# Kernel optimization log

Hardware: AMD Instinct MI355X
Metric: run time of the kernel (lower is better)

Reference implementation:

```python
import jax, jax.numpy as jnp
import numpy as np

C, H, W = 4, 84, 84
T, B = 64, 32
HID = 512
ZD = 64
SLOPE = 0.01  # nn.LeakyReLU default


def setup_inputs() -> dict:
    key = jax.random.key(0)
    ks = jax.random.split(key, 16)
    f32 = jnp.float32

    def n(k, shape, scale):
        return jax.random.normal(k, shape, f32) * scale

    return {
        "x": jax.random.normal(ks[0], (T * B, C, H, W), f32),
        "done": (jax.random.uniform(ks[1], (T * B,)) < 0.05).astype(f32),
        "h0": jnp.zeros((B, HID), f32),
        "c0": jnp.zeros((B, HID), f32),
        "conv1_w": n(ks[2], (C, C, 5, 5), 0.15),
        "conv1_b": jnp.zeros((C,), f32),
        "conv2_w": n(ks[3], (C, C, 3, 3), 0.2),
        "conv2_b": jnp.zeros((C,), f32),
        "conv3_w": n(ks[4], (C, C, 3, 3), 0.2),
        "conv3_b": jnp.zeros((C,), f32),
        "fc1_w": n(ks[5], (HID, C * H * W), 0.01),
        "fc1_b": jnp.zeros((HID,), f32),
        "fc2_w": n(ks[6], (HID, HID), 0.05),
        "fc2_b": jnp.zeros((HID,), f32),
        "w_ih": n(ks[7], (4 * HID, HID), 0.04),
        "w_hh": n(ks[8], (4 * HID, HID), 0.04),
        "b_ih": jnp.zeros((4 * HID,), f32),
        "b_hh": jnp.zeros((4 * HID,), f32),
        "df_w": n(ks[9], (128, HID), 0.05),
        "df_b": jnp.zeros((128,), f32),
        "disc_w": n(ks[10], (ZD, 128), 0.01),
        "disc_b": jnp.zeros((ZD,), f32),
    }


def _lrelu(x):
    return jax.nn.leaky_relu(x, SLOPE)


def _conv(x, w, b):
    y = jax.lax.conv_general_dilated(
        x, w, window_strides=(1, 1), padding="SAME",
        dimension_numbers=("NCHW", "OIHW", "NCHW"))
    return _lrelu(y + b[None, :, None, None])


def reference(x, done, h0, c0, conv1_w, conv1_b, conv2_w, conv2_b, conv3_w,
              conv3_b, fc1_w, fc1_b, fc2_w, fc2_b, w_ih, w_hh, b_ih, b_hh,
              df_w, df_b, disc_w, disc_b):
    # conv + MLP feature extractor (self.network)
    h = _conv(x, conv1_w, conv1_b)
    h = _conv(h, conv2_w, conv2_b)
    h = _conv(h, conv3_w, conv3_b)
    h = h.reshape(h.shape[0], -1)                      # [T*B, C*H*W]
    h = _lrelu(h @ fc1_w.T + fc1_b)
    h = _lrelu(h @ fc2_w.T + fc2_b)                    # [T*B, 512]

    # env_first=False path: reshape to [T, B, 512]
    hid = h.reshape(T, B, HID)
    d = done.reshape(T, B)

    def step(carry, xs):
        hp, cp = carry
        xt, dt = xs
        mask = (1.0 - dt)[:, None]                     # done-based state reset
        hp = hp * mask
        cp = cp * mask
        gates = xt @ w_ih.T + b_ih + hp @ w_hh.T + b_hh  # [B, 4*HID], order i,f,g,o
        i, f, g, o = jnp.split(gates, 4, axis=-1)
        c = jax.nn.sigmoid(f) * cp + jax.nn.sigmoid(i) * jnp.tanh(g)
        hn = jax.nn.sigmoid(o) * jnp.tanh(c)
        return (hn, c), hn

    (hN, cN), ys = jax.lax.scan(step, (h0, c0), (hid, d))
    feat = ys.reshape(T * B, HID)

    disc_feat = _lrelu(feat @ df_w.T + df_b)           # [T*B, 128]
    logits = disc_feat @ disc_w.T + disc_b             # [T*B, z_dim]
    return logits, hN, cN
```

## Files before the change

### kernel.cpp

```cpp
#include <hip/hip_runtime.h>
#include <math.h>

#define SLOPE 0.01f

typedef __attribute__((ext_vector_type(8))) short bf16x8;
typedef __attribute__((ext_vector_type(4))) float f32x4;
typedef unsigned short ushort_t;

__device__ __forceinline__ float lrelu(float x) {
    return x > 0.f ? x : SLOPE * x;
}

__device__ __forceinline__ unsigned short f2bf(float f) {
    unsigned int u = __float_as_uint(f);
    u += 0x7fffu + ((u >> 16) & 1u);
    return (unsigned short)(u >> 16);
}

__device__ __forceinline__ float bf2f(unsigned short u) {
    return __uint_as_float((unsigned int)u << 16);
}

__global__ void cvt_bf16_kernel(const float* __restrict__ src,
                                unsigned short* __restrict__ dst, int n4) {
    int i = blockIdx.x * blockDim.x + threadIdx.x;
    if (i >= n4) return;
    float4 v = ((const float4*)src)[i];
    uint2 o;
    o.x = (unsigned)f2bf(v.x) | ((unsigned)f2bf(v.y) << 16);
    o.y = (unsigned)f2bf(v.z) | ((unsigned)f2bf(v.w) << 16);
    ((uint2*)dst)[i] = o;
}

template<int K, bool INBF, bool OUTBF>
__global__ __launch_bounds__(256) void conv_tile_kernel(
        const void* __restrict__ in_v,
        const float* __restrict__ w,
        const float* __restrict__ b,
        void* __restrict__ out_v) {
    constexpr int HALO = K / 2;
    constexpr int TILE_H = 12;
    constexpr int SH = TILE_H + 2 * HALO;
    constexpr int SW = 88;
    __shared__ float smem[4][SH][SW];

    int tid = threadIdx.x;
    int n = blockIdx.x;
    int row0 = blockIdx.y * TILE_H;
    const size_t imgOff = (size_t)n * (4 * 84 * 84);

    for (int it = tid; it < 4 * SH * 22; it += 256) {
        int item = it % 22;
        int rr = it / 22;
        int r = rr % SH;
        int ci = rr / SH;
        int gr = row0 + r - HALO;
        bool rv = (unsigned)gr < 84u;
        if (item < 21) {
            int gc = item * 4;
            float4 v = make_float4(0.f, 0.f, 0.f, 0.f);
            if (rv) {
                size_t off = imgOff + ((size_t)ci * 84 + gr) * 84 + gc;
                if (INBF) {
                    unsigned long long u =
                        *(const unsigned long long*)((const ushort_t*)in_v + off);
                    v.x = bf2f((unsigned short)u);
                    v.y = bf2f((unsigned short)(u >> 16));
                    v.z = bf2f((unsigned short)(u >> 32));
                    v.w = bf2f((unsigned short)(u >> 48));
                } else {
                    v = *(const float4*)((const float*)in_v + off);
                }
            }
            smem[ci][r][HALO + gc + 0] = v.x;
            smem[ci][r][HALO + gc + 1] = v.y;
            smem[ci][r][HALO + gc + 2] = v.z;
            smem[ci][r][HALO + gc + 3] = v.w;
        } else {
            if (HALO == 2) {
                smem[ci][r][0] = 0.f; smem[ci][r][1] = 0.f;
                smem[ci][r][86] = 0.f; smem[ci][r][87] = 0.f;
            } else {
                smem[ci][r][0] = 0.f;
                smem[ci][r][85] = 0.f; smem[ci][r][86] = 0.f; smem[ci][r][87] = 0.f;
            }
        }
    }
    __syncthreads();

    if (tid >= 252) return;
    int r  = tid / 21;
    int w0 = (tid % 21) * 4;

    float acc[4][4];
    #pragma unroll
    for (int co = 0; co < 4; ++co) {
        float bv = b[co];
        #pragma unroll
        for (int dw = 0; dw < 4; ++dw) acc[co][dw] = bv;
    }

    #pragma unroll
    for (int ci = 0; ci < 4; ++ci) {
        #pragma unroll
        for (int kh = 0; kh < K; ++kh) {
            float vals[K + 3];
            float4 v0 = *(const float4*)&smem[ci][r + kh][w0];
            vals[0] = v0.x; vals[1] = v0.y; vals[2] = v0.z; vals[3] = v0.w;
            if (K == 5) {
                float4 v1 = *(const float4*)&smem[ci][r + kh][w0 + 4];
                vals[4] = v1.x; vals[5] = v1.y; vals[6] = v1.z; vals[7] = v1.w;
            } else {
                float2 v1 = *(const float2*)&smem[ci][r + kh][w0 + 4];
                vals[4] = v1.x; vals[5] = v1.y;
            }
            #pragma unroll
            for (int co = 0; co < 4; ++co) {
                #pragma unroll
                for (int kw = 0; kw < K; ++kw) {
                    float wv = w[((co * 4 + ci) * K + kh) * K + kw];
                    #pragma unroll
                    for (int dw = 0; dw < 4; ++dw)
                        acc[co][dw] += vals[kw + dw] * wv;
                }
            }
        }
    }

    int oh = row0 + r;
    #pragma unroll
    for (int co = 0; co < 4; ++co) {
        size_t off = imgOff + ((size_t)co * 84 + oh) * 84 + w0;
        float o0 = lrelu(acc[co][0]);
        float o1 = lrelu(acc[co][1]);
        float o2 = lrelu(acc[co][2]);
        float o3 = lrelu(acc[co][3]);
        if (OUTBF) {
            uint2 p;
            p.x = (unsigned)f2bf(o0) | ((unsigned)f2bf(o1) << 16);
            p.y = (unsigned)f2bf(o2) | ((unsigned)f2bf(o3) << 16);
            *(uint2*)((ushort_t*)out_v + off) = p;
        } else {
            *(float4*)((float*)out_v + off) = make_float4(o0, o1, o2, o3);
        }
    }
}

template<bool DO_LRELU, bool BIAS2, bool OUTBF>
__global__ void gemm_bf16_kernel(const unsigned short* __restrict__ A,
                                 const unsigned short* __restrict__ B,
                                 const float* __restrict__ bias,
                                 const float* __restrict__ bias2,
                                 void* __restrict__ Cout,
                                 int M, int N, int K) {
    __shared__ unsigned short As[64][40];
    __shared__ unsigned short Bs[64][40];
    int tid = threadIdx.x;
    int rowBase = blockIdx.y * 64;
    int colBase = blockIdx.x * 64;

    int wave = tid >> 6;
    int l    = tid & 63;
    int wr = wave >> 1, wc = wave & 1;
    int lane16 = l & 15;
    int kb = (l >> 4) * 8;

    int sr = tid >> 2;
    int sk = (tid & 3) << 3;
    const unsigned short* Ap = A + (size_t)(rowBase + sr) * K + sk;
    const unsigned short* Bp = B + (size_t)(colBase + sr) * K + sk;

    f32x4 acc[2][2] = {};

    for (int k0 = 0; k0 < K; k0 += 32) {
        float4 av = *(const float4*)(Ap + k0);
        float4 bv = *(const float4*)(Bp + k0);
        __syncthreads();
        *(float4*)(&As[sr][sk]) = av;
        *(float4*)(&Bs[sr][sk]) = bv;
        __syncthreads();
        bf16x8 a0 = *(const bf16x8*)(&As[wr * 32 + lane16][kb]);
        bf16x8 a1 = *(const bf16x8*)(&As[wr * 32 + 16 + lane16][kb]);
        bf16x8 b0 = *(const bf16x8*)(&Bs[wc * 32 + lane16][kb]);
        bf16x8 b1 = *(const bf16x8*)(&Bs[wc * 32 + 16 + lane16][kb]);
        acc[0][0] = __builtin_amdgcn_mfma_f32_16x16x32_bf16(a0, b0, acc[0][0], 0, 0, 0);
        acc[0][1] = __builtin_amdgcn_mfma_f32_16x16x32_bf16(a0, b1, acc[0][1], 0, 0, 0);
        acc[1][0] = __builtin_amdgcn_mfma_f32_16x16x32_bf16(a1, b0, acc[1][0], 0, 0, 0);
        acc[1][1] = __builtin_amdgcn_mfma_f32_16x16x32_bf16(a1, b1, acc[1][1], 0, 0, 0);
    }

    int crow0 = rowBase + wr * 32 + (l >> 4) * 4;
    int ccol0 = colBase + wc * 32 + lane16;
    float bsv[2];
    #pragma unroll
    for (int j = 0; j < 2; ++j) {
        bsv[j] = bias[ccol0 + j * 16];
        if (BIAS2) bsv[j] += bias2[ccol0 + j * 16];
    }
    #pragma unroll
    for (int i = 0; i < 2; ++i) {
        #pragma unroll
        for (int r = 0; r < 4; ++r) {
            int row = crow0 + i * 16 + r;
            #pragma unroll
            for (int j = 0; j < 2; ++j) {
                float v = acc[i][j][r] + bsv[j];
                if (DO_LRELU) v = lrelu(v);
                size_t off = (size_t)row * N + ccol0 + j * 16;
                if (OUTBF) ((unsigned short*)Cout)[off] = f2bf(v);
                else       ((float*)Cout)[off] = v;
            }
        }
    }
}

__global__ void gemm_bf16_splitk_kernel(const unsigned short* __restrict__ A,
                                        const unsigned short* __restrict__ B,
                                        float* __restrict__ part,
                                        int M, int N, int K, int kChunk) {
    __shared__ unsigned short As[64][40];
    __shared__ unsigned short Bs[64][40];
    int tid = threadIdx.x;
    int rowBase = blockIdx.y * 64;
    int colBase = blockIdx.x * 64;
    int s = blockIdx.z;
    int kStart = s * kChunk;
    int kEnd = kStart + kChunk;

    int wave = tid >> 6;
    int l    = tid & 63;
    int wr = wave >> 1, wc = wave & 1;
    int lane16 = l & 15;
    int kb = (l >> 4) * 8;

    int sr = tid >> 2;
    int sk = (tid & 3) << 3;
    const unsigned short* Ap = A + (size_t)(rowBase + sr) * K + sk;
    const unsigned short* Bp = B + (size_t)(colBase + sr) * K + sk;

    f32x4 acc[2][2] = {};

    for (int k0 = kStart; k0 < kEnd; k0 += 32) {
        float4 av = *(const float4*)(Ap + k0);
        float4 bv = *(const float4*)(Bp + k0);
        __syncthreads();
        *(float4*)(&As[sr][sk]) = av;
        *(float4*)(&Bs[sr][sk]) = bv;
        __syncthreads();
        bf16x8 a0 = *(const bf16x8*)(&As[wr * 32 + lane16][kb]);
        bf16x8 a1 = *(const bf16x8*)(&As[wr * 32 + 16 + lane16][kb]);
        bf16x8 b0 = *(const bf16x8*)(&Bs[wc * 32 + lane16][kb]);
        bf16x8 b1 = *(const bf16x8*)(&Bs[wc * 32 + 16 + lane16][kb]);
        acc[0][0] = __builtin_amdgcn_mfma_f32_16x16x32_bf16(a0, b0, acc[0][0], 0, 0, 0);
        acc[0][1] = __builtin_amdgcn_mfma_f32_16x16x32_bf16(a0, b1, acc[0][1], 0, 0, 0);
        acc[1][0] = __builtin_amdgcn_mfma_f32_16x16x32_bf16(a1, b0, acc[1][0], 0, 0, 0);
        acc[1][1] = __builtin_amdgcn_mfma_f32_16x16x32_bf16(a1, b1, acc[1][1], 0, 0, 0);
    }

    float* Cp = part + (size_t)s * M * N;
    int crow0 = rowBase + wr * 32 + (l >> 4) * 4;
    int ccol0 = colBase + wc * 32 + lane16;
    #pragma unroll
    for (int i = 0; i < 2; ++i)
        #pragma unroll
        for (int r = 0; r < 4; ++r) {
            int row = crow0 + i * 16 + r;
            #pragma unroll
            for (int j = 0; j < 2; ++j)
                Cp[(size_t)row * N + ccol0 + j * 16] = acc[i][j][r];
        }
}

template<int S>
__global__ void splitk_reduce_kernel(const float* __restrict__ part,
                                     const float* __restrict__ bias,
                                     unsigned short* __restrict__ out,
                                     int MN, int N) {
    int i4 = blockIdx.x * blockDim.x + threadIdx.x;
    if (i4 * 4 >= MN) return;
    float4 acc = ((const float4*)part)[i4];
    #pragma unroll
    for (int s = 1; s < S; ++s) {
        float4 p = ((const float4*)(part + (size_t)s * MN))[i4];
        acc.x += p.x; acc.y += p.y; acc.z += p.z; acc.w += p.w;
    }
    int col4 = i4 % (N / 4);
    float4 bv = ((const float4*)bias)[col4];
    float o0 = lrelu(acc.x + bv.x);
    float o1 = lrelu(acc.y + bv.y);
    float o2 = lrelu(acc.z + bv.z);
    float o3 = lrelu(acc.w + bv.w);
    uint2 p;
    p.x = (unsigned)f2bf(o0) | ((unsigned)f2bf(o1) << 16);
    p.y = (unsigned)f2bf(o2) | ((unsigned)f2bf(o3) << 16);
    ((uint2*)out)[i4] = p;
}

__global__ void lstm_init_kernel(const float* __restrict__ h0,
                                 unsigned short* __restrict__ HA,
                                 int* __restrict__ bar) {
    int i = blockIdx.x * blockDim.x + threadIdx.x;
    if (i < 16384) HA[i] = f2bf(h0[i]);
    if (i < 64) bar[i] = 0;
}

__global__ __launch_bounds__(256, 1) void lstm_scan_kernel(
        const unsigned short* __restrict__ whh_b,
        const unsigned short* __restrict__ wih_b,
        const float* __restrict__ bih,
        const float* __restrict__ bhh,
        const unsigned short* __restrict__ HA,
        const float* __restrict__ c0,
        const unsigned short* __restrict__ hfc2,
        const float* __restrict__ done,
        unsigned short* __restrict__ feat,
        float* __restrict__ hN, float* __restrict__ cN,
        int* __restrict__ bar) {
    __shared__ float mds[2048];
    __shared__ float Gs[4][16][17];
    __shared__ unsigned short Hs[16][520];
    __shared__ unsigned short Xh[16][520];

    int tid = threadIdx.x;
    int jt = blockIdx.x >> 1;
    int bt = blockIdx.x & 1;

    for (int i = tid; i < 2048; i += 256) mds[i] = 1.0f - done[i];

    int g = tid >> 6;
    int l = tid & 63;
    int lane16 = l & 15;
    int khi = l >> 4;
    const unsigned short* Wp =
        whh_b + ((size_t)g * 512 + jt * 16 + lane16) * 512 + khi * 8;
    const unsigned short* Wxp =
        wih_b + ((size_t)g * 512 + jt * 16 + lane16) * 512 + khi * 8;
    bf16x8 wreg[16], wxreg[16];
    #pragma unroll
    for (int kk = 0; kk < 16; ++kk) {
        wreg[kk]  = *(const bf16x8*)(Wp + kk * 32);
        wxreg[kk] = *(const bf16x8*)(Wxp + kk * 32);
    }

    int jloc = tid & 15;
    int bloc = tid >> 4;
    int j = jt * 16 + jloc;
    int b = bt * 16 + bloc;
    float c_reg = c0[b * 512 + j];
    float bsv[4];
    #pragma unroll
    for (int gg = 0; gg < 4; ++gg)
        bsv[gg] = bih[gg * 512 + j] + bhh[gg * 512 + j];

    int* mybar = bar + bt * 32;

    {
        const float4* h4 = (const float4*)(HA + bt * 8192);
        const float4* x4 = (const float4*)(hfc2 + bt * 8192);
        #pragma unroll
        for (int u0 = 0; u0 < 4; ++u0) {
            int u = tid + u0 * 256;
            float4 hv = h4[u];
            float4 xv = x4[u];
            *(float4*)&Hs[u >> 6][(u & 63) * 8] = hv;
            *(float4*)&Xh[u >> 6][(u & 63) * 8] = xv;
        }
    }
    __syncthreads();

    for (int t = 0; t < 64; ++t) {
        f32x4 hacc0 = {}, hacc1 = {}, xacc0 = {}, xacc1 = {};
        #pragma unroll
        for (int kk = 0; kk < 16; kk += 2) {
            bf16x8 hb0 = *(const bf16x8*)(&Hs[lane16][khi * 8 + kk * 32]);
            bf16x8 hb1 = *(const bf16x8*)(&Hs[lane16][khi * 8 + kk * 32 + 32]);
            bf16x8 xb0 = *(const bf16x8*)(&Xh[lane16][khi * 8 + kk * 32]);
            bf16x8 xb1 = *(const bf16x8*)(&Xh[lane16][khi * 8 + kk * 32 + 32]);
            hacc0 = __builtin_amdgcn_mfma_f32_16x16x32_bf16(wreg[kk],      hb0, hacc0, 0, 0, 0);
            hacc1 = __builtin_amdgcn_mfma_f32_16x16x32_bf16(wreg[kk + 1],  hb1, hacc1, 0, 0, 0);
            xacc0 = __builtin_amdgcn_mfma_f32_16x16x32_bf16(wxreg[kk],     xb0, xacc0, 0, 0, 0);
            xacc1 = __builtin_amdgcn_mfma_f32_16x16x32_bf16(wxreg[kk + 1], xb1, xacc1, 0, 0, 0);
        }
        f32x4 hacc = hacc0 + hacc1;
        f32x4 xacc = xacc0 + xacc1;
        float mcol = mds[t * 32 + bt * 16 + lane16];
        #pragma unroll
        for (int r = 0; r < 4; ++r)
            Gs[g][khi * 4 + r][lane16] = xacc[r] + mcol * hacc[r];
        __syncthreads();

        float4 xv0, xv1, xv2, xv3;
        if (t < 63) {
            const float4* x4 =
                (const float4*)(hfc2 + (size_t)(t + 1) * 16384 + bt * 8192);
            xv0 = x4[tid];
            xv1 = x4[tid + 256];
            xv2 = x4[tid + 512];
            xv3 = x4[tid + 768];
        }

        int row = t * 32 + b;
        float m = mds[row];
        float ai = bsv[0] + Gs[0][jloc][bloc];
        float af = bsv[1] + Gs[1][jloc][bloc];
        float ag = bsv[2] + Gs[2][jloc][bloc];
        float ao = bsv[3] + Gs[3][jloc][bloc];
        float cp = c_reg * m;
        float si = 1.f / (1.f + __expf(-ai));
        float sf = 1.f / (1.f + __expf(-af));
        float so = 1.f / (1.f + __expf(-ao));
        c_reg = sf * cp + si * tanhf(ag);
        float hn = so * tanhf(c_reg);
        feat[(size_t)row * 512 + j] = f2bf(hn);
        if (t == 63) {
            hN[b * 512 + j] = hn;
            cN[b * 512 + j] = c_reg;
        }

        if (t < 63) {
            *(float4*)&Xh[tid >> 6][(tid & 63) * 8] = xv0;
            {
                int u = tid + 256;
                *(float4*)&Xh[u >> 6][(u & 63) * 8] = xv1;
                u = tid + 512;
                *(float4*)&Xh[u >> 6][(u & 63) * 8] = xv2;
                u = tid + 768;
                *(float4*)&Xh[u >> 6][(u & 63) * 8] = xv3;
            }
            __syncthreads();
            if (tid == 0) {
                int target = (t + 1) * 32;
                __hip_atomic_fetch_add(mybar, 1, __ATOMIC_ACQ_REL,
                                       __HIP_MEMORY_SCOPE_AGENT);
                while (__hip_atomic_load(mybar, __ATOMIC_RELAXED,
                                         __HIP_MEMORY_SCOPE_AGENT) < target)
                    __builtin_amdgcn_s_sleep(2);
                __builtin_amdgcn_fence(__ATOMIC_ACQUIRE, "agent");
            }
            __syncthreads();
            const float4* h4 =
                (const float4*)(feat + (size_t)t * 16384 + bt * 8192);
            #pragma unroll
            for (int u0 = 0; u0 < 4; ++u0) {
                int u = tid + u0 * 256;
                float4 hv = h4[u];
                *(float4*)&Hs[u >> 6][(u & 63) * 8] = hv;
            }
            __syncthreads();
        }
    }
}

extern "C" void kernel_launch(void* const* d_in, const int* in_sizes, int n_in,
                              void* d_out, int out_size, void* d_ws, size_t ws_size,
                              hipStream_t stream) {
    const float* x    = (const float*)d_in[0];
    const float* done = (const float*)d_in[1];
    const float* h0   = (const float*)d_in[2];
    const float* c0   = (const float*)d_in[3];
    const float* c1w  = (const float*)d_in[4];
    const float* c1b  = (const float*)d_in[5];
    const float* c2w  = (const float*)d_in[6];
    const float* c2b  = (const float*)d_in[7];
    const float* c3w  = (const float*)d_in[8];
    const float* c3b  = (const float*)d_in[9];
    const float* fc1w = (const float*)d_in[10];
    const float* fc1b = (const float*)d_in[11];
    const float* fc2w = (const float*)d_in[12];
    const float* fc2b = (const float*)d_in[13];
    const float* wih  = (const float*)d_in[14];
    const float* whh  = (const float*)d_in[15];
    const float* bih  = (const float*)d_in[16];
    const float* bhh  = (const float*)d_in[17];
    const float* dfw  = (const float*)d_in[18];
    const float* dfb  = (const float*)d_in[19];
    const float* dw   = (const float*)d_in[20];
    const float* db   = (const float*)d_in[21];
    float* out = (float*)d_out;

    const size_t CONV_ELEMS = 57802752;
    char* S = (char*)d_ws;
    unsigned short* c1out  = (unsigned short*)S;   S += CONV_ELEMS * 2;
    unsigned short* c2out  = (unsigned short*)S;   S += CONV_ELEMS * 2;
    unsigned short* c3out  = (unsigned short*)S;   S += CONV_ELEMS * 2;
    unsigned short* fc1w_b = (unsigned short*)S;   S += 28901376;
    unsigned short* fc2w_b = (unsigned short*)S;   S += 524288;
    unsigned short* wih_b  = (unsigned short*)S;   S += 2097152;
    unsigned short* whh_b  = (unsigned short*)S;   S += 2097152;
    unsigned short* dfw_b  = (unsigned short*)S;   S += 131072;
    unsigned short* dw_b   = (unsigned short*)S;   S += 16384;
    unsigned short* hfc1_b = (unsigned short*)S;   S += 2097152;
    unsigned short* hfc2_b = (unsigned short*)S;   S += 2097152;
    unsigned short* feat_b = (unsigned short*)S;   S += 2097152;
    unsigned short* dfeat_b= (unsigned short*)S;   S += 524288;
    unsigned short* HA     = (unsigned short*)S;   S += 32768;
    float*          part   = (float*)S;            S += 37748736;
    int*            bar    = (int*)S;              S += 256;

    dim3 cgrid(2048, 7);
    conv_tile_kernel<5, false, true><<<cgrid, 256, 0, stream>>>(x,     c1w, c1b, c1out);
    conv_tile_kernel<3, true,  true><<<cgrid, 256, 0, stream>>>(c1out, c2w, c2b, c2out);
    conv_tile_kernel<3, true,  true><<<cgrid, 256, 0, stream>>>(c2out, c3w, c3b, c3out);

    auto cvt = [&](const float* s, unsigned short* d, int n) {
        int n4 = n / 4;
        cvt_bf16_kernel<<<(n4 + 255) / 256, 256, 0, stream>>>(s, d, n4);
    };
    cvt(fc1w, fc1w_b, 14450688);
    cvt(fc2w, fc2w_b, 262144);
    cvt(wih,  wih_b,  1048576);
    cvt(whh,  whh_b,  1048576);
    cvt(dfw,  dfw_b,  65536);
    cvt(dw,   dw_b,   8192);

    gemm_bf16_splitk_kernel<<<dim3(8, 32, 9), 256, 0, stream>>>(
        c3out, fc1w_b, part, 2048, 512, 28224, 3136);
    splitk_reduce_kernel<9><<<dim3(1024), 256, 0, stream>>>(
        part, fc1b, hfc1_b, 1048576, 512);

    gemm_bf16_kernel<true, false, true><<<dim3(8, 32), 256, 0, stream>>>(
        hfc1_b, fc2w_b, fc2b, nullptr, hfc2_b, 2048, 512, 512);

    lstm_init_kernel<<<dim3(64), 256, 0, stream>>>(h0, HA, bar);
    lstm_scan_kernel<<<dim3(64), 256, 0, stream>>>(
        whh_b, wih_b, bih, bhh, HA, c0, hfc2_b, done, feat_b,
        out + 131072, out + 131072 + 16384, bar);

    gemm_bf16_kernel<true, false, true><<<dim3(2, 32), 256, 0, stream>>>(
        feat_b, dfw_b, dfb, nullptr, dfeat_b, 2048, 128, 512);
    gemm_bf16_kernel<false, false, false><<<dim3(1, 32), 256, 0, stream>>>(
        dfeat_b, dw_b, db, nullptr, out, 2048, 64, 128);
}
```

Before: 837.0 us.

## Fuse conv2 and conv3 into one tiled kernel and merge weight conversions

```diff
diff --git a/kernel.cpp b/kernel.cpp
--- a/kernel.cpp
+++ b/kernel.cpp
@@ -21,11 +21,23 @@
     return __uint_as_float((unsigned int)u << 16);
 }
 
-__global__ void cvt_bf16_kernel(const float* __restrict__ src,
-                                unsigned short* __restrict__ dst, int n4) {
+__global__ void cvt_all_kernel(const float* __restrict__ s0,
+                               const float* __restrict__ s1,
+                               const float* __restrict__ s2,
+                               const float* __restrict__ s3,
+                               const float* __restrict__ s4,
+                               const float* __restrict__ s5,
+                               unsigned short* __restrict__ dst) {
     int i = blockIdx.x * blockDim.x + threadIdx.x;
-    if (i >= n4) return;
-    float4 v = ((const float4*)src)[i];
+    if (i >= 4220928) return;
+    const float* src; int base;
+    if (i < 3612672)      { src = s0; base = 0; }
+    else if (i < 3678208) { src = s1; base = 3612672; }
+    else if (i < 3940352) { src = s2; base = 3678208; }
+    else if (i < 4202496) { src = s3; base = 3940352; }
+    else if (i < 4218880) { src = s4; base = 4202496; }
+    else                  { src = s5; base = 4218880; }
+    float4 v = ((const float4*)src)[i - base];
     uint2 o;
     o.x = (unsigned)f2bf(v.x) | ((unsigned)f2bf(v.y) << 16);
     o.y = (unsigned)f2bf(v.z) | ((unsigned)f2bf(v.w) << 16);
@@ -142,6 +154,139 @@
             *(uint2*)((ushort_t*)out_v + off) = p;
         } else {
             *(float4*)((float*)out_v + off) = make_float4(o0, o1, o2, o3);
+        }
+    }
+}
+
+__global__ __launch_bounds__(384) void conv23_fused_kernel(
+        const ushort_t* __restrict__ in_b,
+        const float* __restrict__ w2, const float* __restrict__ b2,
+        const float* __restrict__ w3, const float* __restrict__ b3,
+        unsigned short* __restrict__ out) {
+    __shared__ float ins[4][18][88];
+    __shared__ float mid[4][16][88];
+
+    int tid = threadIdx.x;
+    int n = blockIdx.x;
+    int r0 = blockIdx.y * 14;
+    const size_t imgOff = (size_t)n * (4 * 84 * 84);
+
+    for (int it = tid; it < 4 * 18 * 22; it += 384) {
+        int item = it % 22;
+        int rr = it / 22;
+        int r = rr % 18;
+        int ci = rr / 18;
+        int gr = r0 - 2 + r;
+        bool rv = (unsigned)gr < 84u;
+        if (item < 21) {
+            int gc = item * 4;
+            float4 v = make_float4(0.f, 0.f, 0.f, 0.f);
+            if (rv) {
+                unsigned long long u = *(const unsigned long long*)
+                    (in_b + imgOff + ((size_t)ci * 84 + gr) * 84 + gc);
+                v.x = bf2f((unsigned short)u);
+                v.y = bf2f((unsigned short)(u >> 16));
+                v.z = bf2f((unsigned short)(u >> 32));
+                v.w = bf2f((unsigned short)(u >> 48));
+            }
+            ins[ci][r][1 + gc + 0] = v.x;
+            ins[ci][r][1 + gc + 1] = v.y;
+            ins[ci][r][1 + gc + 2] = v.z;
+            ins[ci][r][1 + gc + 3] = v.w;
+        } else {
+            ins[ci][r][0] = 0.f;
+            ins[ci][r][85] = 0.f; ins[ci][r][86] = 0.f; ins[ci][r][87] = 0.f;
+        }
+    }
+    __syncthreads();
+
+    if (tid < 128) {
+        int co = tid >> 5; int rr = (tid & 31) >> 1; int cc = (tid & 1) ? 85 : 0;
+        mid[co][rr][cc] = 0.f;
+    }
+    if (tid < 336) {
+        int m  = tid / 21;
+        int c0 = (tid % 21) * 4;
+        int gm = r0 - 1 + m;
+        float acc[4][4];
+        #pragma unroll
+        for (int co = 0; co < 4; ++co) {
+            float bv = b2[co];
+            #pragma unroll
+            for (int dw = 0; dw < 4; ++dw) acc[co][dw] = bv;
+        }
+        #pragma unroll
+        for (int ci = 0; ci < 4; ++ci) {
+            #pragma unroll
+            for (int kh = 0; kh < 3; ++kh) {
+                float vals[6];
+                float4 v0 = *(const float4*)&ins[ci][m + kh][c0];
+                float2 v1 = *(const float2*)&ins[ci][m + kh][c0 + 4];
+                vals[0] = v0.x; vals[1] = v0.y; vals[2] = v0.z; vals[3] = v0.w;
+                vals[4] = v1.x; vals[5] = v1.y;
+                #pragma unroll
+                for (int co = 0; co < 4; ++co) {
+                    #pragma unroll
+                    for (int kw = 0; kw < 3; ++kw) {
+                        float wv = w2[((co * 4 + ci) * 3 + kh) * 3 + kw];
+                        #pragma unroll
+                        for (int dw = 0; dw < 4; ++dw)
+                            acc[co][dw] += vals[kw + dw] * wv;
+                    }
+                }
+            }
+        }
+        bool valid = (unsigned)gm < 84u;
+        #pragma unroll
+        for (int co = 0; co < 4; ++co)
+            #pragma unroll
+            for (int dw = 0; dw < 4; ++dw)
+                mid[co][m][1 + c0 + dw] = valid ? lrelu(acc[co][dw]) : 0.f;
+    }
+    __syncthreads();
+
+    if (tid < 294) {
+        int ro = tid / 21;
+        int c0 = (tid % 21) * 4;
+        float acc[4][4];
+        #pragma unroll
+        for (int co = 0; co < 4; ++co) {
+            float bv = b3[co];
+            #pragma unroll
+            for (int dw = 0; dw < 4; ++dw) acc[co][dw] = bv;
+        }
+        #pragma unroll
+        for (int ci = 0; ci < 4; ++ci) {
+            #pragma unroll
+            for (int kh = 0; kh < 3; ++kh) {
+                float vals[6];
+                float4 v0 = *(const float4*)&mid[ci][ro + kh][c0];
+                float2 v1 = *(const float2*)&mid[ci][ro + kh][c0 + 4];
+                vals[0] = v0.x; vals[1] = v0.y; vals[2] = v0.z; vals[3] = v0.w;
+                vals[4] = v1.x; vals[5] = v1.y;
+                #pragma unroll
+                for (int co = 0; co < 4; ++co) {
+                    #pragma unroll
+                    for (int kw = 0; kw < 3; ++kw) {
+                        float wv = w3[((co * 4 + ci) * 3 + kh) * 3 + kw];
+                        #pragma unroll
+                        for (int dw = 0; dw < 4; ++dw)
+                            acc[co][dw] += vals[kw + dw] * wv;
+                    }
+                }
+            }
+        }
+        int go = r0 + ro;
+        #pragma unroll
+        for (int co = 0; co < 4; ++co) {
+            float o0 = lrelu(acc[co][0]);
+            float o1 = lrelu(acc[co][1]);
+            float o2 = lrelu(acc[co][2]);
+            float o3 = lrelu(acc[co][3]);
+            uint2 p;
+            p.x = (unsigned)f2bf(o0) | ((unsigned)f2bf(o1) << 16);
+            p.y = (unsigned)f2bf(o2) | ((unsigned)f2bf(o3) << 16);
+            *(uint2*)(out + imgOff + ((size_t)co * 84 + go) * 84 + c0) = p;
         }
     }
 }
@@ -481,7 +626,6 @@
     const size_t CONV_ELEMS = 57802752;
     char* S = (char*)d_ws;
     unsigned short* c1out  = (unsigned short*)S;   S += CONV_ELEMS * 2;
-    unsigned short* c2out  = (unsigned short*)S;   S += CONV_ELEMS * 2;
     unsigned short* c3out  = (unsigned short*)S;   S += CONV_ELEMS * 2;
     unsigned short* fc1w_b = (unsigned short*)S;   S += 28901376;
     unsigned short* fc2w_b = (unsigned short*)S;   S += 524288;
@@ -497,21 +641,13 @@
     float*          part   = (float*)S;            S += 37748736;
     int*            bar    = (int*)S;              S += 256;
 
-    dim3 cgrid(2048, 7);
-    conv_tile_kernel<5, false, true><<<cgrid, 256, 0, stream>>>(x,     c1w, c1b, c1out);
-    conv_tile_kernel<3, true,  true><<<cgrid, 256, 0, stream>>>(c1out, c2w, c2b, c2out);
-    conv_tile_kernel<3, true,  true><<<cgrid, 256, 0, stream>>>(c2out, c3w, c3b, c3out);
-
-    auto cvt = [&](const float* s, unsigned short* d, int n) {
-        int n4 = n / 4;
-        cvt_bf16_kernel<<<(n4 + 255) / 256, 256, 0, stream>>>(s, d, n4);
-    };
-    cvt(fc1w, fc1w_b, 14450688);
-    cvt(fc2w, fc2w_b, 262144);
-    cvt(wih,  wih_b,  1048576);
-    cvt(whh,  whh_b,  1048576);
-    cvt(dfw,  dfw_b,  65536);
-    cvt(dw,   dw_b,   8192);
+    conv_tile_kernel<5, false, true><<<dim3(2048, 7), 256, 0, stream>>>(
+        x, c1w, c1b, c1out);
+    conv23_fused_kernel<<<dim3(2048, 6), 384, 0, stream>>>(
+        c1out, c2w, c2b, c3w, c3b, c3out);
+
+    cvt_all_kernel<<<dim3((4220928 + 255) / 256), 256, 0, stream>>>(
+        fc1w, fc2w, wih, whh, dfw, dw, fc1w_b);
 
     gemm_bf16_splitk_kernel<<<dim3(8, 32, 9), 256, 0, stream>>>(
         c3out, fc1w_b, part, 2048, 512, 28224, 3136);
```

After: 1.049 ms. 1.25x slower.
